# Optimization experiments

Hardware: AMD Instinct MI355X
Metric: run time of the kernel (lower is better)

## Reference

```python
import jax, jax.numpy as jnp
import numpy as np

INPUT_SIZE = 500
SENTENCE_SIZE = 128


def setup_inputs() -> dict:
    key = jax.random.key(0)
    ks = jax.random.split(key, 20)
    B, D = 16, 512
    Ho, Hi, Hu = 4, 4, 4
    dh_ori = D // Ho          # 128
    dh = D // (Hi + Hu)       # 64
    s = 0.05
    code = jax.random.normal(ks[0], (B, INPUT_SIZE, D), jnp.float32)
    # binary sentence-membership mask (which code tokens belong to each sentence)
    input_sentence = (jax.random.uniform(ks[1], (B, SENTENCE_SIZE, INPUT_SIZE)) < 0.2).astype(jnp.float32)

    def W(k, h, dout):
        return jax.random.normal(k, (h, D, dout), jnp.float32) * s

    def b(k, h, dout):
        return jax.random.normal(k, (h, dout), jnp.float32) * 0.01

    return dict(
        code=code, input_sentence=input_sentence,
        Wq_ori=W(ks[2], Ho, dh_ori), bq_ori=b(ks[3], Ho, dh_ori),
        Wk_ori=W(ks[4], Ho, dh_ori), bk_ori=b(ks[5], Ho, dh_ori),
        Wq_in=W(ks[6], Hi, dh), bq_in=b(ks[7], Hi, dh),
        Wk_in=W(ks[8], Hi, dh), bk_in=b(ks[9], Hi, dh),
        Wv_in=W(ks[10], Hi, dh), bv_in=b(ks[11], Hi, dh),
        Wq_out=W(ks[12], Hu, dh), bq_out=b(ks[13], Hu, dh),
        Wk_out=W(ks[14], Hu, dh), bk_out=b(ks[15], Hu, dh),
        Wv_out=W(ks[16], Hu, dh), bv_out=b(ks[17], Hu, dh),
    )


def _proj(x, W, b):
    # x: (B, N, D), W: (H, D, F), b: (H, F) -> (B, H, N, F), relu Dense per head
    return jax.nn.relu(jnp.einsum('bnd,hdf->bhnf', x, W) + b[:, None, :])


def reference(code, input_sentence,
              Wq_ori, bq_ori, Wk_ori, bk_ori,
              Wq_in, bq_in, Wk_in, bk_in, Wv_in, bv_in,
              Wq_out, bq_out, Wk_out, bk_out, Wv_out, bv_out):
    B, S = input_sentence.shape[0], input_sentence.shape[1]
    sent = input_sentence

    # ---- original (ori) branch: max over heads of raw QK^T, mask, matmul code ----
    q = _proj(code, Wq_ori, bq_ori)
    k = _proj(code, Wk_ori, bk_ori)
    scores_ori = jnp.einsum('bhnf,bhmf->bhnm', q, k).max(axis=1)      # (B, N, N)
    sA = jnp.einsum('bsn,bnm->bsm', sent, scores_ori)                 # (B, S, N)
    out_ori = jnp.einsum('bsm,bmd->bsd', sent * sA, code)             # (B, S, D)

    # ---- in-mask heads ----
    qi = _proj(code, Wq_in, bq_in)
    ki = _proj(code, Wk_in, bk_in)
    vi = _proj(code, Wv_in, bv_in)
    sc = jnp.einsum('bhnf,bhmf->bhnm', qi, ki)                        # (B, Hi, N, N)
    sAi = jnp.einsum('bsn,bhnm->bhsm', sent, sc)                      # (B, Hi, S, N)
    out_in = jnp.einsum('bhsm,bhmf->bhsf', sent[:, None] * sAi, vi)   # (B, Hi, S, F)

    # ---- out-mask heads ----
    qo = _proj(code, Wq_out, bq_out)
    ko = _proj(code, Wk_out, bk_out)
    vo = _proj(code, Wv_out, bv_out)
    sco = jnp.einsum('bhnf,bhmf->bhnm', qo, ko)
    sAo = jnp.einsum('bsn,bhnm->bhsm', sent, sco)
    masked = (sent - 1.0)[:, None] * sAo                              # (B, Hu, S, N)
    include = sent.sum(axis=2)[:, None, :, None]                      # (B, 1, S, 1)
    masked = masked / (INPUT_SIZE - include) * include
    out_out = jnp.einsum('bhsm,bhmf->bhsf', masked, vo)               # (B, Hu, S, F)

    # original returns a list [ori, in_0..in_Hi-1, out_0..out_Hu-1]; concat along features
    in_flat = jnp.transpose(out_in, (0, 2, 1, 3)).reshape(B, S, -1)
    out_flat = jnp.transpose(out_out, (0, 2, 1, 3)).reshape(B, S, -1)
    return jnp.concatenate([out_ori, in_flat, out_flat], axis=-1)
```

## Files before the change

### kernel.cpp

```cpp
#include <hip/hip_runtime.h>
#include <cfloat>

#define B_  16
#define N_  500
#define NP  512
#define S_  128
#define D_  512
#define FO  128
#define FI  64

typedef unsigned short u16;
typedef __attribute__((ext_vector_type(8))) short bf8;
typedef __attribute__((ext_vector_type(4))) float f4;

#define MFMA(a,b,c) __builtin_amdgcn_mfma_f32_16x16x32_bf16((a),(b),(c),0,0,0)

__device__ __forceinline__ u16 f2b(float x){
    union{float f;unsigned u;} v; v.f=x;
    unsigned r = v.u + 0x7fffu + ((v.u>>16)&1u);
    return (u16)(r>>16);
}
__device__ __forceinline__ float b2f(u16 x){
    union{unsigned u;float f;} v; v.u=((unsigned)x)<<16; return v.f;
}
__device__ __forceinline__ bf8 ldb8(const u16* p){ return *(const bf8*)p; }

__device__ __forceinline__ void gl2lds16(const u16* g, u16* lds){
    __builtin_amdgcn_global_load_lds(
        (const __attribute__((address_space(1))) unsigned int*)g,
        (__attribute__((address_space(3))) unsigned int*)lds, 16, 0, 0);
}
__device__ __forceinline__ void vdrain(){
    asm volatile("s_waitcnt vmcnt(0)" ::: "memory");
}

__global__ __launch_bounds__(256) void prep_code(const float* __restrict__ code,
                                                 u16* __restrict__ codeB,
                                                 u16* __restrict__ codeT)
{
    __shared__ float T[64][65];
    const int b = blockIdx.x, m0 = blockIdx.y*64, d0 = blockIdx.z*64;
    const int t = threadIdx.x;
    #pragma unroll
    for (int i=0;i<16;++i){
        int idx = t + i*256; int rr = idx>>6, cc = idx&63;
        int m = m0+rr;
        T[rr][cc] = (m < N_) ? code[((size_t)b*N_+m)*D_ + d0+cc] : 0.f;
    }
    __syncthreads();
    #pragma unroll
    for (int i=0;i<16;++i){
        int idx=t+i*256; int rr=idx>>6, cc=idx&63; int m=m0+rr;
        if (m<N_) codeB[((size_t)b*N_+m)*D_ + d0+cc] = f2b(T[rr][cc]);
    }
    #pragma unroll
    for (int i=0;i<16;++i){
        int idx=t+i*256; int dd=idx>>6, mm=idx&63;
        codeT[((size_t)b*D_ + d0+dd)*NP + m0+mm] = f2b(T[mm][dd]);
    }
}

__global__ __launch_bounds__(128) void prep_sent(const float* __restrict__ sent,
                                                 u16* __restrict__ sentB,
                                                 float* __restrict__ inc)
{
    const int b=blockIdx.x, s=blockIdx.y, t=threadIdx.x;
    const float* row = sent + ((size_t)b*S_+s)*N_;
    float4 v = make_float4(0.f,0.f,0.f,0.f);
    const int n = t*4;
    if (n < N_) v = *(const float4*)(row+n);
    float sum = v.x+v.y+v.z+v.w;
    ushort4 o; o.x=f2b(v.x); o.y=f2b(v.y); o.z=f2b(v.z); o.w=f2b(v.w);
    *(ushort4*)&sentB[((size_t)b*S_+s)*NP + n] = o;
    #pragma unroll
    for (int off=32; off; off>>=1) sum += __shfl_down(sum, off);
    __shared__ float ls[2];
    if ((t&63)==0) ls[t>>6]=sum;
    __syncthreads();
    if (t==0) inc[b*S_+s] = ls[0]+ls[1];
}

struct PWAll { const float* W[8]; u16* WT[8]; };
__global__ __launch_bounds__(256) void prep_w_all(PWAll a)
{
    const int slot = blockIdx.y;
    const int widx = slot<4 ? (slot>>1) : slot-2;
    const int ftile= slot<4 ? (slot&1)  : 0;
    const int F    = slot<4 ? 128 : 64;
    const float* W = a.W[widx];
    u16* WT        = a.WT[widx];
    __shared__ float T[64][65];
    const int h=blockIdx.x, f0=ftile*64, d0=blockIdx.z*64, t=threadIdx.x;
    #pragma unroll
    for (int i=0;i<16;++i){
        int idx=t+i*256; int rr=idx>>6, cc=idx&63;
        T[rr][cc] = W[((size_t)h*D_ + d0+rr)*F + f0+cc];
    }
    __syncthreads();
    #pragma unroll
    for (int i=0;i<16;++i){
        int idx=t+i*256; int ff=idx>>6, dd=idx&63;
        WT[((size_t)h*F + f0+ff)*D_ + d0+dd] = f2b(T[dd][ff]);
    }
}

__global__ __launch_bounds__(256) void zero_pad4(u16* a0, u16* a1, u16* a2, u16* a3)
{
    u16* arr4[4] = {a0,a1,a2,a3};
    u16* base = arr4[blockIdx.y] + (size_t)blockIdx.x*FI*NP;
    for (int idx=threadIdx.x; idx<FI*12; idx+=256){
        int f = idx/12, n = N_ + idx%12;
        base[(size_t)f*NP + n] = 0;
    }
}

struct GemmOut { const float* bias[8]; u16* dst[8]; };
union ProjLDS {
    u16 ab[4][4096];
    u16 ot[16896];
};
__global__ __launch_bounds__(256) void proj_gemm(const u16* __restrict__ codeB,
                                                 const u16* __restrict__ WallT,
                                                 GemmOut go)
{
    __shared__ alignas(16) ProjLDS L;

    const int t = threadIdx.x;
    const int w = t>>6, l = t&63, lane16 = l&15, lq = l>>4;
    const int bid = blockIdx.x;
    const int xcd = bid & 7;
    const int g   = bid >> 3;
    const int rt  = xcd*8 + g/20;
    const int ct  = g - (g/20)*20;
    const int r0 = rt*128;
    const int c0 = ct*128;
    const int wr = (w>>1)*64, wc = (w&1)*64;
    const int srow = l>>2;
    const int scol = (l&3)*8;

    f4 acc[4][4] = {};

    auto STAGE = [&](u16* Ad, u16* Bd, int k0){
        #pragma unroll
        for (int iss=0; iss<2; ++iss){
            const int rbase = w*32 + iss*16;
            gl2lds16(codeB + (size_t)(r0+rbase+srow)*D_ + k0 + scol, Ad + rbase*32);
            gl2lds16(WallT + (size_t)(c0+rbase+srow)*D_ + k0 + scol, Bd + rbase*32);
        }
    };
    auto COMPUTE = [&](const u16* Ad, const u16* Bd){
        bf8 af[4], bfr[4];
        #pragma unroll
        for (int i=0;i<4;++i){
            af[i]  = *(const bf8*)&Ad[(wr + i*16 + lane16)*32 + lq*8];
            bfr[i] = *(const bf8*)&Bd[(wc + i*16 + lane16)*32 + lq*8];
        }
        #pragma unroll
        for (int i=0;i<4;++i)
            #pragma unroll
            for (int j=0;j<4;++j)
                acc[i][j] = MFMA(af[i], bfr[j], acc[i][j]);
    };

    STAGE(L.ab[0], L.ab[2], 0);
    #pragma unroll
    for (int k0=0; k0<D_; k0+=64){
        vdrain(); __syncthreads();
        if (k0+32 < D_) STAGE(L.ab[1], L.ab[3], k0+32);
        COMPUTE(L.ab[0], L.ab[2]);
        vdrain(); __syncthreads();
        if (k0+64 < D_) STAGE(L.ab[0], L.ab[2], k0+64);
        COMPUTE(L.ab[1], L.ab[3]);
    }

    const int ri = (ct<4) ? 0 : (ct<8) ? 1 : 2 + ((ct-8)>>1);
    const bool tr = (ri==2)||(ri==4)||(ri==5)||(ri==7);

    vdrain(); __syncthreads();

    #pragma unroll
    for (int j=0;j<4;++j){
        const int c = c0 + wc + j*16 + lane16;
        const int idx = (c < 1024) ? (c & 511) : ((c-1024) & 255);
        const float bv = go.bias[ri][idx];
        if (tr){
            #pragma unroll
            for (int i=0;i<4;++i){
                ushort4 o4;
                float x0=acc[i][j][0]+bv, x1=acc[i][j][1]+bv, x2=acc[i][j][2]+bv, x3=acc[i][j][3]+bv;
                o4.x=f2b(x0>0.f?x0:0.f); o4.y=f2b(x1>0.f?x1:0.f);
                o4.z=f2b(x2>0.f?x2:0.f); o4.w=f2b(x3>0.f?x3:0.f);
                *(ushort4*)&L.ot[(wc+j*16+lane16)*132 + wr+i*16+lq*4] = o4;
            }
        } else {
            #pragma unroll
            for (int i=0;i<4;++i)
                #pragma unroll
                for (int reg=0;reg<4;++reg){
                    float x = acc[i][j][reg] + bv;
                    L.ot[(wr+i*16+lq*4+reg)*132 + wc+j*16+lane16] = f2b(x>0.f?x:0.f);
                }
        }
    }
    __syncthreads();

    if (tr){
        const int c  = t>>1;
        const int cg = c0 + c;
        const int u  = cg - 1024;
        const int hfv = u & 255, h = hfv>>6, f2 = hfv & 63;
        u16* dbase = go.dst[ri];
        const int half = t & 1;
        #pragma unroll
        for (int k2=0;k2<16;++k2){
            const int r  = half*64 + k2*4;
            const int rb = r0 + r;
            if (rb < 8000){
                const int b = rb/500, n = rb - b*500;
                *(ushort4*)&dbase[((size_t)(b*4+h)*FI + f2)*NP + n] =
                    *(const ushort4*)&L.ot[c*132 + r];
            }
        }
    } else {
        const int r  = t>>1;
        const int rb = r0 + r;
        if (rb < 8000){
            const int b = rb/500, n = rb - b*500;
            const int half = t & 1;
            const int cg0 = c0 + half*64;
            int h, f2base, F2;
            if (cg0 < 1024){ const int hf0 = cg0 & 511; h = hf0>>7; f2base = hf0 & 127; F2 = 128; }
            else           { const int hf0 = (cg0-1024) & 255; h = hf0>>6; f2base = hf0 & 63; F2 = 64; }
            u16* dstp = go.dst[ri] + ((size_t)(b*4+h)*N_ + n)*F2 + f2base;
            #pragma unroll
            for (int k2=0;k2<16;++k2)
                *(ushort4*)&dstp[k2*4] = *(const ushort4*)&L.ot[r*132 + half*64 + k2*4];
        }
    }
}

__global__ __launch_bounds__(256) void ms_mfma(const u16* __restrict__ q,
                                               const u16* __restrict__ k,
                                               u16* __restrict__ maxscT)
{
    __shared__ alignas(16) u16 Qs[64][136];
    __shared__ alignas(16) u16 Ks[128][136];
    const int t=threadIdx.x, w=t>>6, l=t&63, lane16=l&15, lq=l>>4;
    const int b=blockIdx.x, n0=blockIdx.y*64, m0=blockIdx.z*128;
    const int wr=(w>>1)*32, wc=(w&1)*64;

    f4 best[2][4];
    #pragma unroll
    for(int rt=0;rt<2;++rt)
        #pragma unroll
        for(int ct=0;ct<4;++ct)
            #pragma unroll
            for(int i=0;i<4;++i) best[rt][ct][i] = -FLT_MAX;

    for (int h=0;h<4;++h){
        const u16* qh = q + (size_t)(b*4+h)*N_*FO;
        const u16* kh = k + (size_t)(b*4+h)*N_*FO;
        #pragma unroll
        for (int i=0;i<4;++i){
            const int e=t+i*256, row=e>>4, kc=(e&15)*8;
            int n=n0+row; if(n>N_-1)n=N_-1;
            *(bf8*)&Qs[row][kc] = ldb8(qh + (size_t)n*FO + kc);
        }
        #pragma unroll
        for (int i=0;i<8;++i){
            const int e=t+i*256, row=e>>4, kc=(e&15)*8;
            int m=m0+row; if(m>N_-1)m=N_-1;
            *(bf8*)&Ks[row][kc] = ldb8(kh + (size_t)m*FO + kc);
        }
        __syncthreads();
        f4 acc[2][4]={};
        #pragma unroll
        for (int kk=0;kk<FO;kk+=32){
            bf8 a0=*(const bf8*)&Qs[wr+lane16][kk+lq*8];
            bf8 a1=*(const bf8*)&Qs[wr+16+lane16][kk+lq*8];
            #pragma unroll
            for(int ct=0;ct<4;++ct){
                bf8 bb=*(const bf8*)&Ks[wc+ct*16+lane16][kk+lq*8];
                acc[0][ct]=MFMA(a0,bb,acc[0][ct]);
                acc[1][ct]=MFMA(a1,bb,acc[1][ct]);
            }
        }
        #pragma unroll
        for(int rt=0;rt<2;++rt)
            #pragma unroll
            for(int ct=0;ct<4;++ct)
                #pragma unroll
                for(int i=0;i<4;++i) best[rt][ct][i] = fmaxf(best[rt][ct][i], acc[rt][ct][i]);
        __syncthreads();
    }
    #pragma unroll
    for(int rt=0;rt<2;++rt)
        #pragma unroll
        for(int ct=0;ct<4;++ct){
            const int m  = m0+wc+ct*16+lane16;
            const int nb = n0+wr+rt*16+lq*4;
            ushort4 o; o.x=f2b(best[rt][ct][0]); o.y=f2b(best[rt][ct][1]);
            o.z=f2b(best[rt][ct][2]); o.w=f2b(best[rt][ct][3]);
            *(ushort4*)&maxscT[((size_t)b*NP+m)*NP + nb] = o;
        }
}

__global__ __launch_bounds__(512) void saoo(const u16* __restrict__ sentB,
                                            const u16* __restrict__ maxscT,
                                            const u16* __restrict__ codeT,
                                            float* __restrict__ out)
{
    __shared__ u16 sAmS[16][520];
    const int b=blockIdx.x, s0=blockIdx.y*16;
    const int t=threadIdx.x, w=t>>6, l=t&63, lane16=l&15, lq=l>>4;

    {
        const int m0 = w*64;
        const u16* ap = sentB + ((size_t)b*S_ + s0+lane16)*NP + lq*8;
        const u16* bp[4];
        #pragma unroll
        for(int ct=0;ct<4;++ct) bp[ct] = maxscT + ((size_t)b*NP + m0+ct*16+lane16)*NP + lq*8;
        f4 acc[4] = {};
        for (int k0=0;k0<NP;k0+=32){
            bf8 av=ldb8(ap+k0);
            #pragma unroll
            for(int ct=0;ct<4;++ct) acc[ct]=MFMA(av, ldb8(bp[ct]+k0), acc[ct]);
        }
        #pragma unroll
        for(int ct=0;ct<4;++ct){
            const int m = m0+ct*16+lane16;
            #pragma unroll
            for(int reg=0;reg<4;++reg){
                const int s = s0+lq*4+reg;
                const float sv = b2f(sentB[((size_t)b*S_+s)*NP+m]);
                sAmS[lq*4+reg][m] = (sv != 0.f) ? f2b(acc[ct][reg]*sv) : (u16)0;
            }
        }
    }
    __syncthreads();
    {
        const int d0 = w*64;
        const u16* bp[4];
        #pragma unroll
        for(int ct=0;ct<4;++ct) bp[ct] = codeT + ((size_t)b*D_ + d0+ct*16+lane16)*NP + lq*8;
        f4 acc[4] = {};
        for (int k0=0;k0<NP;k0+=32){
            bf8 av = *(const bf8*)&sAmS[lane16][k0+lq*8];
            #pragma unroll
            for(int ct=0;ct<4;++ct) acc[ct]=MFMA(av, ldb8(bp[ct]+k0), acc[ct]);
        }
        #pragma unroll
        for(int ct=0;ct<4;++ct){
            const int d = d0+ct*16+lane16;
            #pragma unroll
            for(int reg=0;reg<4;++reg){
                const int s = s0+lq*4+reg;
                out[((size_t)b*S_+s)*1024 + d] = acc[ct][reg];
            }
        }
    }
}

struct AttnArgs { const u16* qT[2]; const u16* kp[2]; const u16* vT[2]; };
__global__ __launch_bounds__(256) void attn_fused(AttnArgs a,
                                                  const u16* __restrict__ sentB,
                                                  const float* __restrict__ inc,
                                                  float* __restrict__ out)
{
    __shared__ float red[4][32][68];
    __shared__ u16 qsS[32][72];
    __shared__ u16 Pw[4][32][72];
    const int bh=blockIdx.x, b=bh>>2, h=bh&3, s0=blockIdx.y*32, br=blockIdx.z;
    const u16* qT = a.qT[br];
    const u16* kp = a.kp[br];
    const u16* vT = a.vT[br];
    const int t=threadIdx.x, w=t>>6, l=t&63, lane16=l&15, lq=l>>4;

    {
        const u16 *ap[2], *bp[4];
        #pragma unroll
        for(int rt=0;rt<2;++rt) ap[rt] = sentB + ((size_t)b*S_ + s0+rt*16+lane16)*NP + w*128 + lq*8;
        #pragma unroll
        for(int ct=0;ct<4;++ct) bp[ct] = qT + ((size_t)bh*FI + ct*16+lane16)*NP + w*128 + lq*8;
        f4 acc[2][4] = {};
        #pragma unroll
        for (int k0=0;k0<128;k0+=32){
            bf8 a0=ldb8(ap[0]+k0), a1=ldb8(ap[1]+k0);
            #pragma unroll
            for(int ct=0;ct<4;++ct){
                bf8 bb=ldb8(bp[ct]+k0);
                acc[0][ct]=MFMA(a0,bb,acc[0][ct]);
                acc[1][ct]=MFMA(a1,bb,acc[1][ct]);
            }
        }
        #pragma unroll
        for(int rt=0;rt<2;++rt)
            #pragma unroll
            for(int ct=0;ct<4;++ct)
                #pragma unroll
                for(int reg=0;reg<4;++reg)
                    red[w][rt*16+lq*4+reg][ct*16+lane16] = acc[rt][ct][reg];
    }
    __syncthreads();
    {
        const int s=t>>3, f0=(t&7)*8;
        #pragma unroll
        for (int j=0;j<8;++j){
            float v = red[0][s][f0+j]+red[1][s][f0+j]+red[2][s][f0+j]+red[3][s][f0+j];
            qsS[s][f0+j] = f2b(v);
        }
    }
    __syncthreads();

    f4 accO[2][4] = {};
    #pragma unroll
    for (int c=0;c<2;++c){
        const int m0 = w*64 + c*256;
        f4 p[2][4] = {};
        const u16* bp[4];
        #pragma unroll
        for(int ct=0;ct<4;++ct){
            int m=m0+ct*16+lane16; if(m>N_-1)m=N_-1;
            bp[ct] = kp + ((size_t)bh*N_+m)*FI + lq*8;
        }
        #pragma unroll
        for (int kk=0; kk<FI; kk+=32){
            bf8 a0 = *(const bf8*)&qsS[lane16][kk+lq*8];
            bf8 a1 = *(const bf8*)&qsS[16+lane16][kk+lq*8];
            #pragma unroll
            for(int ct=0;ct<4;++ct){
                bf8 bb=ldb8(bp[ct]+kk);
                p[0][ct]=MFMA(a0,bb,p[0][ct]);
                p[1][ct]=MFMA(a1,bb,p[1][ct]);
            }
        }
        #pragma unroll
        for(int rt=0;rt<2;++rt)
            #pragma unroll
            for(int ct=0;ct<4;++ct){
                const int m = m0+ct*16+lane16;
                #pragma unroll
                for(int reg=0;reg<4;++reg){
                    const int s = s0+rt*16+lq*4+reg;
                    const float sv = b2f(sentB[((size_t)b*S_+s)*NP+m]);
                    const float wgt = br ? ((m<N_)? sv-1.f : 0.f) : sv;
                    Pw[w][rt*16+lq*4+reg][ct*16+lane16] = f2b(p[rt][ct][reg]*wgt);
                }
            }
        #pragma unroll
        for (int kk2=0; kk2<64; kk2+=32){
            bf8 a2[2];
            #pragma unroll
            for(int rt=0;rt<2;++rt) a2[rt] = *(const bf8*)&Pw[w][rt*16+lane16][kk2+lq*8];
            #pragma unroll
            for(int ct=0;ct<4;++ct){
                bf8 vv = ldb8(vT + ((size_t)bh*FI + ct*16+lane16)*NP + m0+kk2+lq*8);
                accO[0][ct]=MFMA(a2[0],vv,accO[0][ct]);
                accO[1][ct]=MFMA(a2[1],vv,accO[1][ct]);
            }
        }
    }
    #pragma unroll
    for(int rt=0;rt<2;++rt)
        #pragma unroll
        for(int ct=0;ct<4;++ct)
            #pragma unroll
            for(int reg=0;reg<4;++reg)
                red[w][rt*16+lq*4+reg][ct*16+lane16] = accO[rt][ct][reg];
    __syncthreads();
    {
        const int s=t>>3, f0=(t&7)*8;
        float fac = 1.f;
        if (br){ const float ic = inc[b*S_+s0+s]; fac = ic/(500.f-ic); }
        const size_t o = ((size_t)b*S_+s0+s)*1024 + (br?768:512) + h*FI + f0;
        #pragma unroll
        for (int j=0;j<8;++j){
            float v = red[0][s][f0+j]+red[1][s][f0+j]+red[2][s][f0+j]+red[3][s][f0+j];
            out[o+j] = v*fac;
        }
    }
}

extern "C" void kernel_launch(void* const* d_in, const int* in_sizes, int n_in,
                              void* d_out, int out_size, void* d_ws, size_t ws_size,
                              hipStream_t stream)
{
    const float* code   = (const float*)d_in[0];
    const float* sent   = (const float*)d_in[1];
    const float* Wq_ori = (const float*)d_in[2];
    const float* bq_ori = (const float*)d_in[3];
    const float* Wk_ori = (const float*)d_in[4];
    const float* bk_ori = (const float*)d_in[5];
    const float* Wq_in  = (const float*)d_in[6];
    const float* bq_in  = (const float*)d_in[7];
    const float* Wk_in  = (const float*)d_in[8];
    const float* bk_in  = (const float*)d_in[9];
    const float* Wv_in  = (const float*)d_in[10];
    const float* bv_in  = (const float*)d_in[11];
    const float* Wq_out = (const float*)d_in[12];
    const float* bq_out = (const float*)d_in[13];
    const float* Wk_out = (const float*)d_in[14];
    const float* bk_out = (const float*)d_in[15];
    const float* Wv_out = (const float*)d_in[16];
    const float* bv_out = (const float*)d_in[17];
    float* out = (float*)d_out;

    char* w = (char*)d_ws;
    u16*   codeB  = (u16*)(w);
    u16*   WallT  = (u16*)(w + 8388608);
    u16*   WTqo   = WallT;
    u16*   WTko   = WallT +  262144;
    u16*   WTqi   = WallT +  524288;
    u16*   WTki   = WallT +  655360;
    u16*   WTvi   = WallT +  786432;
    u16*   WTqu   = WallT +  917504;
    u16*   WTku   = WallT + 1048576;
    u16*   WTvu   = WallT + 1179648;
    u16*   sentB  = (u16*)(w + 11010048);
    float* incp   = (float*)(w + 13107200);
    u16* q_ori  = (u16*)(w + 13115392);
    u16* k_ori  = (u16*)(w + 21307392);
    u16* maxscT = (u16*)(w + 29499392);
    u16* codeT  = (u16*)(w + 37888000);
    u16* k_in   = (u16*)(w + 46276608);
    u16* k_out  = (u16*)(w + 50372608);
    u16* qT_in  = (u16*)(w + 54468608);
    u16* qT_out = (u16*)(w + 58662912);
    u16* vT_in  = (u16*)(w + 62857216);
    u16* vT_out = (u16*)(w + 67051520);

    prep_code<<<dim3(16,8,8), 256, 0, stream>>>(code, codeB, codeT);
    prep_sent<<<dim3(16,128), 128, 0, stream>>>(sent, sentB, incp);
    PWAll pw;
    pw.W[0]=Wq_ori; pw.W[1]=Wk_ori; pw.W[2]=Wq_in; pw.W[3]=Wk_in;
    pw.W[4]=Wv_in;  pw.W[5]=Wq_out; pw.W[6]=Wk_out; pw.W[7]=Wv_out;
    pw.WT[0]=WTqo; pw.WT[1]=WTko; pw.WT[2]=WTqi; pw.WT[3]=WTki;
    pw.WT[4]=WTvi; pw.WT[5]=WTqu; pw.WT[6]=WTku; pw.WT[7]=WTvu;
    prep_w_all<<<dim3(4,10,8), 256, 0, stream>>>(pw);
    zero_pad4<<<dim3(64,4), 256, 0, stream>>>(qT_in, qT_out, vT_in, vT_out);

    GemmOut go;
    go.bias[0]=bq_ori; go.bias[1]=bk_ori; go.bias[2]=bq_in; go.bias[3]=bk_in;
    go.bias[4]=bv_in;  go.bias[5]=bq_out; go.bias[6]=bk_out; go.bias[7]=bv_out;
    go.dst[0]=q_ori; go.dst[1]=k_ori; go.dst[2]=qT_in; go.dst[3]=k_in;
    go.dst[4]=vT_in; go.dst[5]=qT_out; go.dst[6]=k_out; go.dst[7]=vT_out;
    proj_gemm<<<dim3(1280), 256, 0, stream>>>(codeB, WallT, go);

    ms_mfma<<<dim3(16,8,4), 256, 0, stream>>>(q_ori, k_ori, maxscT);
    saoo<<<dim3(16,8), 512, 0, stream>>>(sentB, maxscT, codeT, out);

    AttnArgs aa;
    aa.qT[0]=qT_in;  aa.qT[1]=qT_out;
    aa.kp[0]=k_in;   aa.kp[1]=k_out;
    aa.vT[0]=vT_in;  aa.vT[1]=vT_out;
    attn_fused<<<dim3(64,4,2), 256, 0, stream>>>(aa, sentB, incp, out);
}
```

Before: 139.5 us.

## Merge prep kernels into two launches and swizzle proj_gemm LDS layout

Folds the four preprocessing kernels (code cast/transpose, weight transpose, sentence cast plus row sums, pad zeroing) into two launches that pick their role from a flattened block index. The aim is to cut launch overhead and the tail idle time between small kernels. Separately, the projection GEMM now XOR-swizzles the 16-byte column groups in its LDS tiles on both the async global-to-LDS store and the fragment reads, to reduce LDS bank conflicts. The swizzle only works if the global-to-LDS placement lines up with the permuted source columns, so a mismatch would give wrong results.

```diff
diff --git a/kernel.cpp b/kernel.cpp
--- a/kernel.cpp
+++ b/kernel.cpp
@@ -34,83 +34,94 @@
     asm volatile("s_waitcnt vmcnt(0)" ::: "memory");
 }
 
-__global__ __launch_bounds__(256) void prep_code(const float* __restrict__ code,
-                                                 u16* __restrict__ codeB,
-                                                 u16* __restrict__ codeT)
+struct PWAll { const float* W[8]; u16* WT[8]; };
+__global__ __launch_bounds__(256) void prep_all(const float* __restrict__ code,
+                                                u16* __restrict__ codeB,
+                                                u16* __restrict__ codeT,
+                                                PWAll a)
 {
     __shared__ float T[64][65];
-    const int b = blockIdx.x, m0 = blockIdx.y*64, d0 = blockIdx.z*64;
     const int t = threadIdx.x;
-    #pragma unroll
-    for (int i=0;i<16;++i){
-        int idx = t + i*256; int rr = idx>>6, cc = idx&63;
-        int m = m0+rr;
-        T[rr][cc] = (m < N_) ? code[((size_t)b*N_+m)*D_ + d0+cc] : 0.f;
-    }
-    __syncthreads();
-    #pragma unroll
-    for (int i=0;i<16;++i){
-        int idx=t+i*256; int rr=idx>>6, cc=idx&63; int m=m0+rr;
-        if (m<N_) codeB[((size_t)b*N_+m)*D_ + d0+cc] = f2b(T[rr][cc]);
-    }
-    #pragma unroll
-    for (int i=0;i<16;++i){
-        int idx=t+i*256; int dd=idx>>6, mm=idx&63;
-        codeT[((size_t)b*D_ + d0+dd)*NP + m0+mm] = f2b(T[mm][dd]);
-    }
-}
-
-__global__ __launch_bounds__(128) void prep_sent(const float* __restrict__ sent,
-                                                 u16* __restrict__ sentB,
-                                                 float* __restrict__ inc)
-{
-    const int b=blockIdx.x, s=blockIdx.y, t=threadIdx.x;
-    const float* row = sent + ((size_t)b*S_+s)*N_;
-    float4 v = make_float4(0.f,0.f,0.f,0.f);
-    const int n = t*4;
-    if (n < N_) v = *(const float4*)(row+n);
-    float sum = v.x+v.y+v.z+v.w;
-    ushort4 o; o.x=f2b(v.x); o.y=f2b(v.y); o.z=f2b(v.z); o.w=f2b(v.w);
-    *(ushort4*)&sentB[((size_t)b*S_+s)*NP + n] = o;
-    #pragma unroll
-    for (int off=32; off; off>>=1) sum += __shfl_down(sum, off);
-    __shared__ float ls[2];
-    if ((t&63)==0) ls[t>>6]=sum;
-    __syncthreads();
-    if (t==0) inc[b*S_+s] = ls[0]+ls[1];
-}
-
-struct PWAll { const float* W[8]; u16* WT[8]; };
-__global__ __launch_bounds__(256) void prep_w_all(PWAll a)
-{
-    const int slot = blockIdx.y;
-    const int widx = slot<4 ? (slot>>1) : slot-2;
-    const int ftile= slot<4 ? (slot&1)  : 0;
-    const int F    = slot<4 ? 128 : 64;
-    const float* W = a.W[widx];
-    u16* WT        = a.WT[widx];
-    __shared__ float T[64][65];
-    const int h=blockIdx.x, f0=ftile*64, d0=blockIdx.z*64, t=threadIdx.x;
-    #pragma unroll
-    for (int i=0;i<16;++i){
-        int idx=t+i*256; int rr=idx>>6, cc=idx&63;
-        T[rr][cc] = W[((size_t)h*D_ + d0+rr)*F + f0+cc];
-    }
-    __syncthreads();
-    #pragma unroll
-    for (int i=0;i<16;++i){
-        int idx=t+i*256; int ff=idx>>6, dd=idx&63;
-        WT[((size_t)h*F + f0+ff)*D_ + d0+dd] = f2b(T[dd][ff]);
-    }
-}
-
-__global__ __launch_bounds__(256) void zero_pad4(u16* a0, u16* a1, u16* a2, u16* a3)
-{
-    u16* arr4[4] = {a0,a1,a2,a3};
-    u16* base = arr4[blockIdx.y] + (size_t)blockIdx.x*FI*NP;
-    for (int idx=threadIdx.x; idx<FI*12; idx+=256){
-        int f = idx/12, n = N_ + idx%12;
-        base[(size_t)f*NP + n] = 0;
+    const int x = blockIdx.x;
+    if (x < 1024){
+        const int b  = x >> 6;
+        const int m0 = ((x >> 3) & 7) * 64;
+        const int d0 = (x & 7) * 64;
+        #pragma unroll
+        for (int i=0;i<16;++i){
+            int idx = t + i*256; int rr = idx>>6, cc = idx&63;
+            int m = m0+rr;
+            T[rr][cc] = (m < N_) ? code[((size_t)b*N_+m)*D_ + d0+cc] : 0.f;
+        }
+        __syncthreads();
+        #pragma unroll
+        for (int i=0;i<16;++i){
+            int idx=t+i*256; int rr=idx>>6, cc=idx&63; int m=m0+rr;
+            if (m<N_) codeB[((size_t)b*N_+m)*D_ + d0+cc] = f2b(T[rr][cc]);
+        }
+        #pragma unroll
+        for (int i=0;i<16;++i){
+            int idx=t+i*256; int dd=idx>>6, mm=idx&63;
+            codeT[((size_t)b*D_ + d0+dd)*NP + m0+mm] = f2b(T[mm][dd]);
+        }
+    } else {
+        const int v    = x - 1024;
+        const int h    = v / 80;
+        const int rem  = v - h*80;
+        const int slot = rem >> 3;
+        const int d0   = (rem & 7) * 64;
+        const int widx = slot<4 ? (slot>>1) : slot-2;
+        const int ftile= slot<4 ? (slot&1)  : 0;
+        const int F    = slot<4 ? 128 : 64;
+        const float* W = a.W[widx];
+        u16* WT        = a.WT[widx];
+        const int f0 = ftile*64;
+        #pragma unroll
+        for (int i=0;i<16;++i){
+            int idx=t+i*256; int rr=idx>>6, cc=idx&63;
+            T[rr][cc] = W[((size_t)h*D_ + d0+rr)*F + f0+cc];
+        }
+        __syncthreads();
+        #pragma unroll
+        for (int i=0;i<16;++i){
+            int idx=t+i*256; int ff=idx>>6, dd=idx&63;
+            WT[((size_t)h*F + f0+ff)*D_ + d0+dd] = f2b(T[dd][ff]);
+        }
+    }
+}
+
+__global__ __launch_bounds__(256) void prep_sent_pad(const float* __restrict__ sent,
+                                                     u16* __restrict__ sentB,
+                                                     float* __restrict__ inc,
+                                                     u16* a0, u16* a1, u16* a2, u16* a3)
+{
+    const int t = threadIdx.x;
+    const int x = blockIdx.x;
+    if (x < 1024){
+        const int b  = x >> 6;
+        const int s  = (x & 63)*2 + (t >> 7);
+        const int tl = t & 127;
+        const float* row = sent + ((size_t)b*S_+s)*N_;
+        float4 v = make_float4(0.f,0.f,0.f,0.f);
+        const int n = tl*4;
+        if (n < N_) v = *(const float4*)(row+n);
+        float sum = v.x+v.y+v.z+v.w;
+        ushort4 o; o.x=f2b(v.x); o.y=f2b(v.y); o.z=f2b(v.z); o.w=f2b(v.w);
+        *(ushort4*)&sentB[((size_t)b*S_+s)*NP + n] = o;
+        #pragma unroll
+        for (int off=32; off; off>>=1) sum += __shfl_down(sum, off);
+        __shared__ float ls[4];
+        if ((t&63)==0) ls[t>>6]=sum;
+        __syncthreads();
+        if (tl==0) inc[b*S_+s] = ls[(t>>7)*2] + ls[(t>>7)*2+1];
+    } else {
+        const int u  = x - 1024;
+        u16* arr4[4] = {a0,a1,a2,a3};
+        u16* base = arr4[u>>6] + (size_t)(u&63)*FI*NP;
+        for (int idx=t; idx<FI*12; idx+=256){
+            int f = idx/12, n = N_ + idx%12;
+            base[(size_t)f*NP + n] = 0;
+        }
     }
 }
 
@@ -136,7 +147,6 @@
     const int c0 = ct*128;
     const int wr = (w>>1)*64, wc = (w&1)*64;
     const int srow = l>>2;
-    const int scol = (l&3)*8;
 
     f4 acc[4][4] = {};
 
@@ -144,16 +154,20 @@
         #pragma unroll
         for (int iss=0; iss<2; ++iss){
             const int rbase = w*32 + iss*16;
-            gl2lds16(codeB + (size_t)(r0+rbase+srow)*D_ + k0 + scol, Ad + rbase*32);
-            gl2lds16(WallT + (size_t)(c0+rbase+srow)*D_ + k0 + scol, Bd + rbase*32);
+            const int R  = rbase + srow;
+            const int cg = ((l&3) ^ ((R>>1)&3))*8;
+            gl2lds16(codeB + (size_t)(r0+R)*D_ + k0 + cg, Ad + rbase*32);
+            gl2lds16(WallT + (size_t)(c0+R)*D_ + k0 + cg, Bd + rbase*32);
         }
     };
     auto COMPUTE = [&](const u16* Ad, const u16* Bd){
         bf8 af[4], bfr[4];
         #pragma unroll
         for (int i=0;i<4;++i){
-            af[i]  = *(const bf8*)&Ad[(wr + i*16 + lane16)*32 + lq*8];
-            bfr[i] = *(const bf8*)&Bd[(wc + i*16 + lane16)*32 + lq*8];
+            const int Ra = wr + i*16 + lane16;
+            const int Rb = wc + i*16 + lane16;
+            af[i]  = *(const bf8*)&Ad[Ra*32 + ((lq ^ ((Ra>>1)&3))*8)];
+            bfr[i] = *(const bf8*)&Bd[Rb*32 + ((lq ^ ((Rb>>1)&3))*8)];
         }
         #pragma unroll
         for (int i=0;i<4;++i)
@@ -529,15 +543,14 @@
     u16* vT_in  = (u16*)(w + 62857216);
     u16* vT_out = (u16*)(w + 67051520);
 
-    prep_code<<<dim3(16,8,8), 256, 0, stream>>>(code, codeB, codeT);
-    prep_sent<<<dim3(16,128), 128, 0, stream>>>(sent, sentB, incp);
     PWAll pw;
     pw.W[0]=Wq_ori; pw.W[1]=Wk_ori; pw.W[2]=Wq_in; pw.W[3]=Wk_in;
     pw.W[4]=Wv_in;  pw.W[5]=Wq_out; pw.W[6]=Wk_out; pw.W[7]=Wv_out;
     pw.WT[0]=WTqo; pw.WT[1]=WTko; pw.WT[2]=WTqi; pw.WT[3]=WTki;
     pw.WT[4]=WTvi; pw.WT[5]=WTqu; pw.WT[6]=WTku; pw.WT[7]=WTvu;
-    prep_w_all<<<dim3(4,10,8), 256, 0, stream>>>(pw);
-    zero_pad4<<<dim3(64,4), 256, 0, stream>>>(qT_in, qT_out, vT_in, vT_out);
+    prep_all<<<dim3(1344), 256, 0, stream>>>(code, codeB, codeT, pw);
+    prep_sent_pad<<<dim3(1280), 256, 0, stream>>>(sent, sentB, incp,
+                                                  qT_in, qT_out, vT_in, vT_out);
 
     GemmOut go;
     go.bias[0]=bq_ori; go.bias[1]=bk_ori; go.bias[2]=bq_in; go.bias[3]=bk_in;
```

Result: faster. 133.1 us (-4.6%).
